# Performance work log

Measured on AMD Instinct MI355X. Metric: run time of the kernel, lower is better.

## Reference

```python
import jax, jax.numpy as jnp
import numpy as np

B, MBITS, P = 4096, 64, 64
BLK = P // 8          # 8: block size for crop-robust pattern
FREQ = P // 4         # 16: low-res frequency pattern size
KS, SIGMA = 5, 1.0


def _interp_matrix(n_in, n_out):
    # 1D bilinear interpolation matrix with align_corners=True semantics
    pos = jnp.arange(n_out, dtype=jnp.float32) * (n_in - 1) / (n_out - 1)
    lo = jnp.floor(pos).astype(jnp.int32)
    hi = jnp.minimum(lo + 1, n_in - 1)
    w = pos - lo.astype(jnp.float32)
    rows = jnp.arange(n_out)
    M = jnp.zeros((n_out, n_in), jnp.float32)
    M = M.at[rows, lo].add(1.0 - w).at[rows, hi].add(w)
    return M


def _gaussian_kernel(ks, sigma):
    c = jnp.arange(ks, dtype=jnp.float32) - ks // 2
    g = jnp.exp(-c**2 / (2.0 * sigma**2))
    g = g / g.sum()
    k2 = jnp.outer(g, g)
    return k2 / k2.sum()


def setup_inputs() -> dict:
    key = jax.random.key(0)
    ks = jax.random.split(key, 8)

    def lin(k, fan_in, fan_out):
        lim = 1.0 / np.sqrt(fan_in)
        return jax.random.uniform(k, (fan_in, fan_out), jnp.float32, -lim, lim)

    return {
        'message': jax.random.uniform(ks[0], (B, MBITS), jnp.float32),
        'sW1': lin(ks[1], MBITS, 256), 'sb1': jnp.zeros((256,), jnp.float32),
        'sW2': lin(ks[2], 256, 512),   'sb2': jnp.zeros((512,), jnp.float32),
        'sW3': lin(ks[3], 512, P * P), 'sb3': jnp.zeros((P * P,), jnp.float32),
        'fW1': lin(ks[4], MBITS, 128), 'fb1': jnp.zeros((128,), jnp.float32),
        'fW2': lin(ks[5], 128, FREQ * FREQ), 'fb2': jnp.zeros((FREQ * FREQ,), jnp.float32),
    }


def reference(message, sW1, sb1, sW2, sb2, sW3, sb3, fW1, fb1, fW2, fb2):
    b = message.shape[0]
    # --- spatial pattern: MLP -> tanh -> [B,1,P,P]
    h = jax.nn.relu(message @ sW1 + sb1)
    h = jax.nn.relu(h @ sW2 + sb2)
    spatial = jnp.tanh(h @ sW3 + sb3).reshape(b, 1, P, P)

    # --- frequency pattern: MLP -> tanh -> [B,1,16,16] -> bilinear upsample to PxP
    f = jax.nn.relu(message @ fW1 + fb1)
    freq_lo = jnp.tanh(f @ fW2 + fb2).reshape(b, FREQ, FREQ)
    M = _interp_matrix(FREQ, P)  # [P, FREQ]
    freq = jnp.einsum('ph,bhw,qw->bpq', M, freq_lo, M)[:, None]  # [B,1,P,P]

    # --- block pattern: bit i -> 8x8 block (row-major over an 8x8 grid)
    blocks = message.reshape(b, 8, 8)  # [B, rows, cols] of bits
    block = jnp.repeat(jnp.repeat(blocks, BLK, axis=1), BLK, axis=2)[:, None]  # [B,1,P,P]

    rgb = jnp.concatenate([spatial, freq, block], axis=1)  # [B,3,P,P]

    # --- depthwise 5x5 Gaussian smoothing, groups=3
    k2 = _gaussian_kernel(KS, SIGMA)
    kernel = jnp.broadcast_to(k2, (3, 1, KS, KS))
    out = jax.lax.conv_general_dilated(
        rgb, kernel, window_strides=(1, 1), padding=[(KS // 2, KS // 2)] * 2,
        dimension_numbers=('NCHW', 'OIHW', 'NCHW'), feature_group_count=3)
    return out
```

## Files before the change

kernel.cpp:

```cpp
#include <hip/hip_runtime.h>
#include <math.h>

#define BATCH 4096

typedef __attribute__((ext_vector_type(8))) short short8;
typedef __attribute__((ext_vector_type(4))) float f32x4;

__device__ __forceinline__ unsigned short f2bf(float f) {
  unsigned int u = __float_as_uint(f);
  u += 0x7FFF + ((u >> 16) & 1);
  return (unsigned short)(u >> 16);
}

#define GLL16(g, l)                                                    \
  __builtin_amdgcn_global_load_lds(                                    \
      (const __attribute__((address_space(1))) unsigned int*)(g),      \
      (__attribute__((address_space(3))) unsigned int*)(l), 16, 0, 0)

template <int ACT, int OBF16>
__global__ __launch_bounds__(256) void gemm_act(
    const float* __restrict__ A, const float* __restrict__ B,
    const float* __restrict__ bias, void* __restrict__ Cv,
    int M, int N, int K, int ldc) {
  __shared__ float As[16][68];
  __shared__ float Bs[16][64];

  const int t = threadIdx.x;
  const int bm = blockIdx.x * 64;
  const int bn = blockIdx.y * 64;
  const int tx = t & 15;
  const int ty = t >> 4;

  float acc[4][4] = {};

  for (int k0 = 0; k0 < K; k0 += 16) {
    {
      const int m = t >> 2;
      const int kq = t & 3;
      const float4 av =
          *reinterpret_cast<const float4*>(&A[(size_t)(bm + m) * K + k0 + kq * 4]);
      As[kq * 4 + 0][m] = av.x;
      As[kq * 4 + 1][m] = av.y;
      As[kq * 4 + 2][m] = av.z;
      As[kq * 4 + 3][m] = av.w;
    }
    {
      const int k = t >> 4;
      const int nq = t & 15;
      const float4 bv =
          *reinterpret_cast<const float4*>(&B[(size_t)(k0 + k) * N + bn + nq * 4]);
      *reinterpret_cast<float4*>(&Bs[k][nq * 4]) = bv;
    }
    __syncthreads();

#pragma unroll
    for (int kk = 0; kk < 16; ++kk) {
      float a[4], b[4];
#pragma unroll
      for (int i = 0; i < 4; ++i) a[i] = As[kk][ty * 4 + i];
#pragma unroll
      for (int j = 0; j < 4; ++j) b[j] = Bs[kk][tx * 4 + j];
#pragma unroll
      for (int i = 0; i < 4; ++i)
#pragma unroll
        for (int j = 0; j < 4; ++j) acc[i][j] += a[i] * b[j];
    }
    __syncthreads();
  }

#pragma unroll
  for (int i = 0; i < 4; ++i) {
    const int m = bm + ty * 4 + i;
#pragma unroll
    for (int j = 0; j < 4; ++j) {
      const int n = bn + tx * 4 + j;
      float v = acc[i][j] + bias[n];
      if (ACT == 0)
        v = fmaxf(v, 0.0f);
      else
        v = tanhf(v);
      if (OBF16)
        ((unsigned short*)Cv)[(size_t)m * ldc + n] = f2bf(v);
      else
        ((float*)Cv)[(size_t)m * ldc + n] = v;
    }
  }
}

__global__ __launch_bounds__(256) void transpose_w3(
    const float* __restrict__ W, unsigned short* __restrict__ WT) {
  __shared__ float tile[32][33];
  const int bx = blockIdx.x;
  const int by = blockIdx.y;
  const int t = threadIdx.x;
  {
    const int r = t >> 3, c4 = (t & 7) * 4;
    const float4 v =
        *reinterpret_cast<const float4*>(&W[(size_t)(by * 32 + r) * 4096 + bx * 32 + c4]);
    tile[r][c4 + 0] = v.x;
    tile[r][c4 + 1] = v.y;
    tile[r][c4 + 2] = v.z;
    tile[r][c4 + 3] = v.w;
  }
  __syncthreads();
  {
    const int nl = t >> 3, k4 = (t & 7) * 4;
    unsigned short o[4];
#pragma unroll
    for (int i = 0; i < 4; ++i) o[i] = f2bf(tile[k4 + i][nl]);
    *reinterpret_cast<ushort4*>(&WT[(size_t)(bx * 32 + nl) * 512 + by * 32 + k4]) =
        *reinterpret_cast<const ushort4*>(o);
  }
}

__global__ __launch_bounds__(256) void gemm3_mfma(
    const unsigned short* __restrict__ A, const unsigned short* __restrict__ BT,
    const float* __restrict__ bias, float* __restrict__ out) {
  __shared__ __align__(16) unsigned short As[128 * 32];
  __shared__ __align__(16) unsigned short Bs[128 * 32];

  const int t = threadIdx.x;
  const int lane = t & 63;
  const int w = t >> 6;
  const int bm = blockIdx.x * 128;
  const int bn = blockIdx.y * 128;

  const int r0 = w * 32 + (lane >> 2);
  const int r1 = r0 + 16;
  const int c0 = (lane & 3) ^ ((r0 >> 1) & 3);
  const int c1 = (lane & 3) ^ ((r1 >> 1) & 3);

  const unsigned short* gA0 = A + (size_t)(bm + r0) * 512 + c0 * 8;
  const unsigned short* gA1 = A + (size_t)(bm + r1) * 512 + c1 * 8;
  const unsigned short* gB0 = BT + (size_t)(bn + r0) * 512 + c0 * 8;
  const unsigned short* gB1 = BT + (size_t)(bn + r1) * 512 + c1 * 8;

  unsigned short* lA0 = &As[(w * 2 + 0) * 512];
  unsigned short* lA1 = &As[(w * 2 + 1) * 512];
  unsigned short* lB0 = &Bs[(w * 2 + 0) * 512];
  unsigned short* lB1 = &Bs[(w * 2 + 1) * 512];

  const int wm = (w >> 1) * 64;
  const int wn = (w & 1) * 64;
  const int lr = lane & 15;
  const int lc = lane >> 4;
  int aoff[4], boff[4];
#pragma unroll
  for (int i = 0; i < 4; ++i) {
    const int row = wm + i * 16 + lr;
    aoff[i] = row * 32 + (lc ^ ((row >> 1) & 3)) * 8;
    const int col = wn + i * 16 + lr;
    boff[i] = col * 32 + (lc ^ ((col >> 1) & 3)) * 8;
  }

  f32x4 acc[4][4];
  const f32x4 z = {0.f, 0.f, 0.f, 0.f};
#pragma unroll
  for (int i = 0; i < 4; ++i)
#pragma unroll
    for (int j = 0; j < 4; ++j) acc[i][j] = z;

  for (int kt = 0; kt < 16; ++kt) {
    GLL16(gA0, lA0);
    GLL16(gA1, lA1);
    GLL16(gB0, lB0);
    GLL16(gB1, lB1);
    __syncthreads();

    short8 a[4], b[4];
#pragma unroll
    for (int i = 0; i < 4; ++i) a[i] = *reinterpret_cast<const short8*>(&As[aoff[i]]);
#pragma unroll
    for (int j = 0; j < 4; ++j) b[j] = *reinterpret_cast<const short8*>(&Bs[boff[j]]);

#pragma unroll
    for (int i = 0; i < 4; ++i)
#pragma unroll
      for (int j = 0; j < 4; ++j)
        acc[i][j] =
            __builtin_amdgcn_mfma_f32_16x16x32_bf16(a[i], b[j], acc[i][j], 0, 0, 0);

    __syncthreads();
    gA0 += 32; gA1 += 32; gB0 += 32; gB1 += 32;
  }

  const int base_row = bm + wm + ((lane >> 4) << 2);
  const int base_col = bn + wn + lr;
#pragma unroll
  for (int i = 0; i < 4; ++i) {
#pragma unroll
    for (int j = 0; j < 4; ++j) {
      const int n = base_col + j * 16;
      const float bv = bias[n];
#pragma unroll
      for (int r = 0; r < 4; ++r) {
        const int m = base_row + i * 16 + r;
        out[(size_t)m * 12288 + n] = tanhf(acc[i][j][r] + bv);
      }
    }
  }
}

__global__ __launch_bounds__(256) void finalize_kernel(
    const float* __restrict__ msg, const float* __restrict__ freq_lo,
    float* __restrict__ out) {
  const int b = blockIdx.x;
  const int c = blockIdx.y;
  const int t = threadIdx.x;

  __shared__ float chan[4096];
  __shared__ float tmp[4096];
  __shared__ float fl[256];
  __shared__ float msgs[64];
  __shared__ int lo_tab[64];
  __shared__ float w_tab[64];

  const float g0 = 0.054488684549644346f;
  const float g1 = 0.24420134200323332f;
  const float g2 = 0.4026199468907953f;
  const float g[5] = {g0, g1, g2, g1, g0};

  if (t < 64) {
    msgs[t] = msg[(size_t)b * 64 + t];
    const float pos = (float)t * (15.0f / 63.0f);
    int lo = (int)floorf(pos);
    if (lo > 15) lo = 15;
    lo_tab[t] = lo;
    w_tab[t] = pos - (float)lo;
  }
  fl[t] = freq_lo[(size_t)b * 256 + t];
  __syncthreads();

  const size_t out_base = (size_t)b * 12288;

  if (c == 0) {
    const float4* src = reinterpret_cast<const float4*>(out + out_base);
    float4* dst = reinterpret_cast<float4*>(chan);
    for (int i = t; i < 1024; i += 256) dst[i] = src[i];
  } else if (c == 1) {
    for (int i = t; i < 4096; i += 256) {
      const int p = i >> 6, q = i & 63;
      const int lp = lo_tab[p], lq = lo_tab[q];
      const int hp = lp < 15 ? lp + 1 : 15;
      const int hq = lq < 15 ? lq + 1 : 15;
      const float wp = w_tab[p], wq = w_tab[q];
      const float v00 = fl[lp * 16 + lq], v01 = fl[lp * 16 + hq];
      const float v10 = fl[hp * 16 + lq], v11 = fl[hp * 16 + hq];
      chan[i] = (1.0f - wp) * ((1.0f - wq) * v00 + wq * v01) +
                wp * ((1.0f - wq) * v10 + wq * v11);
    }
  } else {
    for (int i = t; i < 4096; i += 256) {
      const int p = i >> 6, q = i & 63;
      chan[i] = msgs[((p >> 3) << 3) + (q >> 3)];
    }
  }
  __syncthreads();

  for (int i = t; i < 4096; i += 256) {
    const int p = i >> 6, q = i & 63;
    float s = 0.0f;
#pragma unroll
    for (int d = -2; d <= 2; ++d) {
      const int qq = q + d;
      if (qq >= 0 && qq < 64) s += g[d + 2] * chan[p * 64 + qq];
    }
    tmp[i] = s;
  }
  __syncthreads();

  float4* dst = reinterpret_cast<float4*>(out + out_base + (size_t)c * 4096);
  for (int i = t; i < 1024; i += 256) {
    const int p = i >> 4;
    const int q4 = (i & 15) * 4;
    float s0 = 0.f, s1 = 0.f, s2 = 0.f, s3 = 0.f;
#pragma unroll
    for (int d = -2; d <= 2; ++d) {
      const int pp = p + d;
      if (pp >= 0 && pp < 64) {
        const float gg = g[d + 2];
        const int base = pp * 64 + q4;
        s0 += gg * tmp[base + 0];
        s1 += gg * tmp[base + 1];
        s2 += gg * tmp[base + 2];
        s3 += gg * tmp[base + 3];
      }
    }
    float4 v;
    v.x = s0; v.y = s1; v.z = s2; v.w = s3;
    dst[i] = v;
  }
}

extern "C" void kernel_launch(void* const* d_in, const int* in_sizes, int n_in,
                              void* d_out, int out_size, void* d_ws,
                              size_t ws_size, hipStream_t stream) {
  const float* msg = (const float*)d_in[0];
  const float* sW1 = (const float*)d_in[1];
  const float* sb1 = (const float*)d_in[2];
  const float* sW2 = (const float*)d_in[3];
  const float* sb2 = (const float*)d_in[4];
  const float* sW3 = (const float*)d_in[5];
  const float* sb3 = (const float*)d_in[6];
  const float* fW1 = (const float*)d_in[7];
  const float* fb1 = (const float*)d_in[8];
  const float* fW2 = (const float*)d_in[9];
  const float* fb2 = (const float*)d_in[10];

  float* out = (float*)d_out;
  char* wsb = (char*)d_ws;

  float* h1 = (float*)(wsb);
  unsigned short* h2 = (unsigned short*)(wsb + (4 << 20));
  unsigned short* w3T = (unsigned short*)(wsb + (8 << 20));
  float* f1 = (float*)(wsb + (12 << 20));
  float* fl = (float*)(wsb + (14 << 20));

  const dim3 blk(256);

  transpose_w3<<<dim3(128, 16), blk, 0, stream>>>(sW3, w3T);

  gemm_act<0, 0><<<dim3(64, 4), blk, 0, stream>>>(msg, sW1, sb1, h1, BATCH, 256, 64, 256);
  gemm_act<0, 1><<<dim3(64, 8), blk, 0, stream>>>(h1, sW2, sb2, h2, BATCH, 512, 256, 512);
  gemm3_mfma<<<dim3(32, 32), blk, 0, stream>>>(h2, w3T, sb3, out);

  gemm_act<0, 0><<<dim3(64, 2), blk, 0, stream>>>(msg, fW1, fb1, f1, BATCH, 128, 64, 128);
  gemm_act<1, 0><<<dim3(64, 4), blk, 0, stream>>>(f1, fW2, fb2, fl, BATCH, 256, 128, 256);

  finalize_kernel<<<dim3(BATCH, 3), blk, 0, stream>>>(msg, fl, out);
}
```

Measured before the change: 356.5 us.

## Move spatial MLP layers to bf16 MFMA and fuse frequency MLP into one kernel

```diff
diff --git a/kernel.cpp b/kernel.cpp
--- a/kernel.cpp
+++ b/kernel.cpp
@@ -12,110 +12,78 @@
   return (unsigned short)(u >> 16);
 }
 
+__device__ __forceinline__ float bf2f(unsigned short s) {
+  return __uint_as_float(((unsigned int)s) << 16);
+}
+
+__device__ __forceinline__ float fast_tanh(float x) {
+  const float e = __expf(2.0f * x);
+  const float r = __builtin_amdgcn_rcpf(e + 1.0f);
+  return fmaf(-2.0f, r, 1.0f);
+}
+
 #define GLL16(g, l)                                                    \
   __builtin_amdgcn_global_load_lds(                                    \
       (const __attribute__((address_space(1))) unsigned int*)(g),      \
       (__attribute__((address_space(3))) unsigned int*)(l), 16, 0, 0)
 
-template <int ACT, int OBF16>
-__global__ __launch_bounds__(256) void gemm_act(
-    const float* __restrict__ A, const float* __restrict__ B,
-    const float* __restrict__ bias, void* __restrict__ Cv,
-    int M, int N, int K, int ldc) {
-  __shared__ float As[16][68];
-  __shared__ float Bs[16][64];
-
+__global__ __launch_bounds__(256) void prep_kernel(
+    const float* __restrict__ sW1, const float* __restrict__ sW2,
+    const float* __restrict__ sW3, const float* __restrict__ msg,
+    unsigned short* __restrict__ w1T, unsigned short* __restrict__ w2T,
+    unsigned short* __restrict__ w3T, unsigned short* __restrict__ msgb) {
+  const int b = blockIdx.x;
   const int t = threadIdx.x;
-  const int bm = blockIdx.x * 64;
-  const int bn = blockIdx.y * 64;
-  const int tx = t & 15;
-  const int ty = t >> 4;
-
-  float acc[4][4] = {};
-
-  for (int k0 = 0; k0 < K; k0 += 16) {
-    {
-      const int m = t >> 2;
-      const int kq = t & 3;
-      const float4 av =
-          *reinterpret_cast<const float4*>(&A[(size_t)(bm + m) * K + k0 + kq * 4]);
-      As[kq * 4 + 0][m] = av.x;
-      As[kq * 4 + 1][m] = av.y;
-      As[kq * 4 + 2][m] = av.z;
-      As[kq * 4 + 3][m] = av.w;
-    }
-    {
-      const int k = t >> 4;
-      const int nq = t & 15;
-      const float4 bv =
-          *reinterpret_cast<const float4*>(&B[(size_t)(k0 + k) * N + bn + nq * 4]);
-      *reinterpret_cast<float4*>(&Bs[k][nq * 4]) = bv;
-    }
-    __syncthreads();
-
-#pragma unroll
-    for (int kk = 0; kk < 16; ++kk) {
-      float a[4], b[4];
-#pragma unroll
-      for (int i = 0; i < 4; ++i) a[i] = As[kk][ty * 4 + i];
-#pragma unroll
-      for (int j = 0; j < 4; ++j) b[j] = Bs[kk][tx * 4 + j];
-#pragma unroll
-      for (int i = 0; i < 4; ++i)
-#pragma unroll
-        for (int j = 0; j < 4; ++j) acc[i][j] += a[i] * b[j];
-    }
-    __syncthreads();
-  }
-
-#pragma unroll
-  for (int i = 0; i < 4; ++i) {
-    const int m = bm + ty * 4 + i;
-#pragma unroll
-    for (int j = 0; j < 4; ++j) {
-      const int n = bn + tx * 4 + j;
-      float v = acc[i][j] + bias[n];
-      if (ACT == 0)
-        v = fmaxf(v, 0.0f);
-      else
-        v = tanhf(v);
-      if (OBF16)
-        ((unsigned short*)Cv)[(size_t)m * ldc + n] = f2bf(v);
-      else
-        ((float*)Cv)[(size_t)m * ldc + n] = v;
-    }
-  }
-}
-
-__global__ __launch_bounds__(256) void transpose_w3(
-    const float* __restrict__ W, unsigned short* __restrict__ WT) {
-  __shared__ float tile[32][33];
-  const int bx = blockIdx.x;
-  const int by = blockIdx.y;
-  const int t = threadIdx.x;
+
+  if (b >= 2192) {
+    const int i0 = (b - 2192) * 2048 + t * 8;
+    const float4 v0 = *reinterpret_cast<const float4*>(&msg[i0]);
+    const float4 v1 = *reinterpret_cast<const float4*>(&msg[i0 + 4]);
+    short8 o;
+    o[0] = (short)f2bf(v0.x); o[1] = (short)f2bf(v0.y);
+    o[2] = (short)f2bf(v0.z); o[3] = (short)f2bf(v0.w);
+    o[4] = (short)f2bf(v1.x); o[5] = (short)f2bf(v1.y);
+    o[6] = (short)f2bf(v1.z); o[7] = (short)f2bf(v1.w);
+    *reinterpret_cast<short8*>(&msgb[i0]) = o;
+    return;
+  }
+
+  const float* src;
+  unsigned short* dst;
+  int K, N, lgtN, tile;
+  if (b < 16) {
+    src = sW1; dst = w1T; K = 64; N = 256; lgtN = 3; tile = b;
+  } else if (b < 144) {
+    src = sW2; dst = w2T; K = 256; N = 512; lgtN = 4; tile = b - 16;
+  } else {
+    src = sW3; dst = w3T; K = 512; N = 4096; lgtN = 7; tile = b - 144;
+  }
+  const int ty = tile >> lgtN;
+  const int tx = tile & ((1 << lgtN) - 1);
+
+  __shared__ float tl[32][33];
   {
     const int r = t >> 3, c4 = (t & 7) * 4;
     const float4 v =
-        *reinterpret_cast<const float4*>(&W[(size_t)(by * 32 + r) * 4096 + bx * 32 + c4]);
-    tile[r][c4 + 0] = v.x;
-    tile[r][c4 + 1] = v.y;
-    tile[r][c4 + 2] = v.z;
-    tile[r][c4 + 3] = v.w;
+        *reinterpret_cast<const float4*>(&src[(size_t)(ty * 32 + r) * N + tx * 32 + c4]);
+    tl[r][c4 + 0] = v.x; tl[r][c4 + 1] = v.y;
+    tl[r][c4 + 2] = v.z; tl[r][c4 + 3] = v.w;
   }
   __syncthreads();
   {
     const int nl = t >> 3, k4 = (t & 7) * 4;
     unsigned short o[4];
 #pragma unroll
-    for (int i = 0; i < 4; ++i) o[i] = f2bf(tile[k4 + i][nl]);
-    *reinterpret_cast<ushort4*>(&WT[(size_t)(bx * 32 + nl) * 512 + by * 32 + k4]) =
+    for (int i = 0; i < 4; ++i) o[i] = f2bf(tl[k4 + i][nl]);
+    *reinterpret_cast<ushort4*>(&dst[(size_t)(tx * 32 + nl) * K + ty * 32 + k4]) =
         *reinterpret_cast<const ushort4*>(o);
   }
 }
 
-__global__ __launch_bounds__(256) void gemm3_mfma(
+template <int ACT, int OBF16, int KDIM>
+__global__ __launch_bounds__(256) void gemm_mfma(
     const unsigned short* __restrict__ A, const unsigned short* __restrict__ BT,
-    const float* __restrict__ bias, float* __restrict__ out) {
+    const float* __restrict__ bias, void* __restrict__ Cv, int ldc) {
   __shared__ __align__(16) unsigned short As[128 * 32];
   __shared__ __align__(16) unsigned short Bs[128 * 32];
 
@@ -130,10 +98,10 @@
   const int c0 = (lane & 3) ^ ((r0 >> 1) & 3);
   const int c1 = (lane & 3) ^ ((r1 >> 1) & 3);
 
-  const unsigned short* gA0 = A + (size_t)(bm + r0) * 512 + c0 * 8;
-  const unsigned short* gA1 = A + (size_t)(bm + r1) * 512 + c1 * 8;
-  const unsigned short* gB0 = BT + (size_t)(bn + r0) * 512 + c0 * 8;
-  const unsigned short* gB1 = BT + (size_t)(bn + r1) * 512 + c1 * 8;
+  const unsigned short* gA0 = A + (size_t)(bm + r0) * KDIM + c0 * 8;
+  const unsigned short* gA1 = A + (size_t)(bm + r1) * KDIM + c1 * 8;
+  const unsigned short* gB0 = BT + (size_t)(bn + r0) * KDIM + c0 * 8;
+  const unsigned short* gB1 = BT + (size_t)(bn + r1) * KDIM + c1 * 8;
 
   unsigned short* lA0 = &As[(w * 2 + 0) * 512];
   unsigned short* lA1 = &As[(w * 2 + 1) * 512];
@@ -160,7 +128,8 @@
 #pragma unroll
     for (int j = 0; j < 4; ++j) acc[i][j] = z;
 
-  for (int kt = 0; kt < 16; ++kt) {
+#pragma unroll 1
+  for (int kt = 0; kt < KDIM / 32; ++kt) {
     GLL16(gA0, lA0);
     GLL16(gA1, lA1);
     GLL16(gB0, lB0);
@@ -184,7 +153,7 @@
     gA0 += 32; gA1 += 32; gB0 += 32; gB1 += 32;
   }
 
-  const int base_row = bm + wm + ((lane >> 4) << 2);
+  const int base_row = bm + wm + (lc << 2);
   const int base_col = bn + wn + lr;
 #pragma unroll
   for (int i = 0; i < 4; ++i) {
@@ -195,15 +164,63 @@
 #pragma unroll
       for (int r = 0; r < 4; ++r) {
         const int m = base_row + i * 16 + r;
-        out[(size_t)m * 12288 + n] = tanhf(acc[i][j][r] + bv);
+        float v = acc[i][j][r] + bv;
+        v = (ACT == 0) ? fmaxf(v, 0.0f) : fast_tanh(v);
+        if (OBF16)
+          ((unsigned short*)Cv)[(size_t)m * ldc + n] = f2bf(v);
+        else
+          ((float*)Cv)[(size_t)m * ldc + n] = v;
       }
     }
   }
 }
 
+__global__ __launch_bounds__(256) void freq_mlp(
+    const float* __restrict__ msg, const float* __restrict__ fW1,
+    const float* __restrict__ fb1, const float* __restrict__ fW2,
+    const float* __restrict__ fb2, float* __restrict__ fl) {
+  const int row0 = blockIdx.x * 16;
+  const int t = threadIdx.x;
+
+  __shared__ float ms[16 * 64];
+  __shared__ float f1[16][128];
+
+  *reinterpret_cast<float4*>(&ms[t * 4]) =
+      *reinterpret_cast<const float4*>(&msg[(size_t)row0 * 64 + t * 4]);
+  __syncthreads();
+
+  {
+    const int n = t & 127;
+    const int rb = (t >> 7) * 8;
+    float acc[8] = {};
+    for (int k = 0; k < 64; ++k) {
+      const float wv = fW1[k * 128 + n];
+#pragma unroll
+      for (int r = 0; r < 8; ++r) acc[r] += ms[(rb + r) * 64 + k] * wv;
+    }
+    const float bv = fb1[n];
+#pragma unroll
+    for (int r = 0; r < 8; ++r) f1[rb + r][n] = fmaxf(acc[r] + bv, 0.0f);
+  }
+  __syncthreads();
+
+  {
+    float acc[16] = {};
+    for (int k = 0; k < 128; ++k) {
+      const float wv = fW2[k * 256 + t];
+#pragma unroll
+      for (int r = 0; r < 16; ++r) acc[r] += f1[r][k] * wv;
+    }
+    const float bv = fb2[t];
+#pragma unroll
+    for (int r = 0; r < 16; ++r)
+      fl[(size_t)(row0 + r) * 256 + t] = fast_tanh(acc[r] + bv);
+  }
+}
+
 __global__ __launch_bounds__(256) void finalize_kernel(
-    const float* __restrict__ msg, const float* __restrict__ freq_lo,
-    float* __restrict__ out) {
+    const float* __restrict__ msg, const float* __restrict__ fl_in,
+    const unsigned short* __restrict__ spatial, float* __restrict__ out) {
   const int b = blockIdx.x;
   const int c = blockIdx.y;
   const int t = threadIdx.x;
@@ -220,23 +237,26 @@
   const float g2 = 0.4026199468907953f;
   const float g[5] = {g0, g1, g2, g1, g0};
 
-  if (t < 64) {
-    msgs[t] = msg[(size_t)b * 64 + t];
-    const float pos = (float)t * (15.0f / 63.0f);
-    int lo = (int)floorf(pos);
-    if (lo > 15) lo = 15;
-    lo_tab[t] = lo;
-    w_tab[t] = pos - (float)lo;
-  }
-  fl[t] = freq_lo[(size_t)b * 256 + t];
-  __syncthreads();
-
-  const size_t out_base = (size_t)b * 12288;
+  if (c != 0) {
+    if (t < 64) {
+      msgs[t] = msg[(size_t)b * 64 + t];
+      const float pos = (float)t * (15.0f / 63.0f);
+      int lo = (int)floorf(pos);
+      if (lo > 15) lo = 15;
+      lo_tab[t] = lo;
+      w_tab[t] = pos - (float)lo;
+    }
+    fl[t] = fl_in[(size_t)b * 256 + t];
+  }
+  __syncthreads();
 
   if (c == 0) {
-    const float4* src = reinterpret_cast<const float4*>(out + out_base);
-    float4* dst = reinterpret_cast<float4*>(chan);
-    for (int i = t; i < 1024; i += 256) dst[i] = src[i];
+    const short8* sp = reinterpret_cast<const short8*>(spatial + (size_t)b * 4096);
+    for (int v = t; v < 512; v += 256) {
+      const short8 s = sp[v];
+#pragma unroll
+      for (int j = 0; j < 8; ++j) chan[v * 8 + j] = bf2f((unsigned short)s[j]);
+    }
   } else if (c == 1) {
     for (int i = t; i < 4096; i += 256) {
       const int p = i >> 6, q = i & 63;
@@ -269,7 +289,7 @@
   }
   __syncthreads();
 
-  float4* dst = reinterpret_cast<float4*>(out + out_base + (size_t)c * 4096);
+  float4* dst = reinterpret_cast<float4*>(out + (size_t)b * 12288 + (size_t)c * 4096);
   for (int i = t; i < 1024; i += 256) {
     const int p = i >> 4;
     const int q4 = (i & 15) * 4;
@@ -310,22 +330,24 @@
   float* out = (float*)d_out;
   char* wsb = (char*)d_ws;
 
-  float* h1 = (float*)(wsb);
-  unsigned short* h2 = (unsigned short*)(wsb + (4 << 20));
-  unsigned short* w3T = (unsigned short*)(wsb + (8 << 20));
-  float* f1 = (float*)(wsb + (12 << 20));
-  float* fl = (float*)(wsb + (14 << 20));
+  unsigned short* msgb = (unsigned short*)(wsb);
+  unsigned short* w1T  = (unsigned short*)(wsb + (1 << 19));
+  unsigned short* w2T  = (unsigned short*)(wsb + (1 << 20));
+  unsigned short* w3T  = (unsigned short*)(wsb + (2 << 20));
+  unsigned short* h1   = (unsigned short*)(wsb + (8 << 20));
+  unsigned short* h2   = (unsigned short*)(wsb + (12 << 20));
+  unsigned short* spat = (unsigned short*)(wsb + (16 << 20));
+  float* fl            = (float*)(wsb + (48 << 20));
 
   const dim3 blk(256);
 
-  transpose_w3<<<dim3(128, 16), blk, 0, stream>>>(sW3, w3T);
-
-  gemm_act<0, 0><<<dim3(64, 4), blk, 0, stream>>>(msg, sW1, sb1, h1, BATCH, 256, 64, 256);
-  gemm_act<0, 1><<<dim3(64, 8), blk, 0, stream>>>(h1, sW2, sb2, h2, BATCH, 512, 256, 512);
-  gemm3_mfma<<<dim3(32, 32), blk, 0, stream>>>(h2, w3T, sb3, out);
-
-  gemm_act<0, 0><<<dim3(64, 2), blk, 0, stream>>>(msg, fW1, fb1, f1, BATCH, 128, 64, 128);
-  gemm_act<1, 0><<<dim3(64, 4), blk, 0, stream>>>(f1, fW2, fb2, fl, BATCH, 256, 128, 256);
-
-  finalize_kernel<<<dim3(BATCH, 3), blk, 0, stream>>>(msg, fl, out);
-}
+  prep_kernel<<<dim3(2320), blk, 0, stream>>>(sW1, sW2, sW3, msg, w1T, w2T, w3T, msgb);
+
+  gemm_mfma<0, 1, 64><<<dim3(32, 2), blk, 0, stream>>>(msgb, w1T, sb1, h1, 256);
+  gemm_mfma<0, 1, 256><<<dim3(32, 4), blk, 0, stream>>>(h1, w2T, sb2, h2, 512);
+  gemm_mfma<1, 1, 512><<<dim3(32, 32), blk, 0, stream>>>(h2, w3T, sb3, spat, 4096);
+
+  freq_mlp<<<dim3(256), blk, 0, stream>>>(msg, fW1, fb1, fW2, fb2, fl);
+
+  finalize_kernel<<<dim3(BATCH, 3), blk, 0, stream>>>(msg, fl, spat, out);
+}
```

Measured after the change: 345.2 us. -3.2%, faster.
